# Kernel optimization log

Hardware: AMD Instinct MI355X
Metric: run time of the kernel (lower is better)

## Reference

```python
import jax, jax.numpy as jnp
import numpy as np

B, D_IN, D_PROJ, N_CLS = 4096, 4096, 1024, 32
N_CHILD = (32, 64)


def setup_inputs() -> dict:
    key = jax.random.key(0)
    ks = jax.random.split(key, 12)
    std = 2e-05
    inp = {
        "x": jax.random.normal(ks[0], (B, D_IN), dtype=jnp.float32),
        "y": jax.random.randint(ks[1], (B,), 0, N_CLS, dtype=jnp.int32),
        # parent projection: Linear(D_IN, D_PROJ)
        "Wp": jax.random.normal(ks[2], (D_IN, D_PROJ), dtype=jnp.float32) * std,
        "bp": jnp.zeros((D_PROJ,), jnp.float32),
        # subclass projection: Linear(D_IN, D_PROJ)
        "Ws": jax.random.normal(ks[3], (D_IN, D_PROJ), dtype=jnp.float32) * std,
        "bs": jnp.zeros((D_PROJ,), jnp.float32),
        # parent classifier: Linear(D_PROJ, N_CLS)
        "Wc": jax.random.normal(ks[4], (D_PROJ, N_CLS), dtype=jnp.float32) * std,
        "bc": jnp.zeros((N_CLS,), jnp.float32),
        # child expert banks: level i has N_CLS experts of Linear(D_PROJ, N_CHILD[i])
        "cw0": jax.random.normal(ks[5], (N_CLS, N_CHILD[0], D_PROJ), dtype=jnp.float32) * std,
        "cb0": jnp.zeros((N_CLS, N_CHILD[0]), jnp.float32),
        "cw1": jax.random.normal(ks[6], (N_CLS, N_CHILD[1], D_PROJ), dtype=jnp.float32) * std,
        "cb1": jnp.zeros((N_CLS, N_CHILD[1]), jnp.float32),
    }
    return inp


def reference(x, y, Wp, bp, Ws, bs, Wc, bc, cw0, cb0, cw1, cb1):
    # dropout p = 0.0 -> identity
    parent_proj_embed = x @ Wp + bp                 # [B, D_PROJ]
    parent_logits = parent_proj_embed @ Wc + bc     # [B, N_CLS]
    child_proj_embed = x @ Ws + bs                  # [B, D_PROJ]
    # per-sample expert routing: gather the expert for label y[b], then batched matvec
    child_logits0 = jnp.einsum("bd,bnd->bn", child_proj_embed, cw0[y]) + cb0[y]  # [B, 32]
    child_logits1 = jnp.einsum("bd,bnd->bn", child_proj_embed, cw1[y]) + cb1[y]  # [B, 64]
    return (parent_logits, child_logits0, child_logits1, parent_proj_embed, child_proj_embed)
```

## Files before the change

### kernel.cpp

```cpp
#include <hip/hip_runtime.h>
#include <hip/hip_bf16.h>
#include <stdint.h>


typedef __attribute__((ext_vector_type(4))) float  floatx4;
typedef __attribute__((ext_vector_type(8))) short  shortx8;
typedef __attribute__((ext_vector_type(4))) short  shortx4;
typedef __attribute__((ext_vector_type(8))) __bf16 bf16x8;

static __device__ __forceinline__ ushort f32_to_bf16_rne(float f) {
  uint32_t u = __builtin_bit_cast(uint32_t, f);
  u += 0x7FFFu + ((u >> 16) & 1u);
  return (ushort)(u >> 16);
}

static __device__ __forceinline__ void async_copy16(const void* g, void* lds) {
  __builtin_amdgcn_global_load_lds(
      (__attribute__((address_space(1))) void*)(uintptr_t)g,
      (__attribute__((address_space(3))) void*)(uintptr_t)lds,
      16, 0, 0);
}

__global__ __launch_bounds__(256) void k_prep(
    const float* __restrict__ x,   const int* __restrict__ y,
    const float* __restrict__ Wp,  const float* __restrict__ Ws,
    const float* __restrict__ Wc,
    const float* __restrict__ cw0, const float* __restrict__ cw1,
    ushort* __restrict__ xb,  ushort* __restrict__ Bt1,
    ushort* __restrict__ cwb, ushort* __restrict__ Wcb,
    int* __restrict__ perm, int* __restrict__ offs)
{
  __shared__ __align__(16) ushort tile[64 * 72];
  __shared__ int hist[32], hbase[32], hcur[32];
  const int b = blockIdx.x;
  const int t = threadIdx.x;

  if (b == 0) {
    if (t < 32) { hist[t] = 0; hcur[t] = 0; }
    __syncthreads();
    int yv[16];
    #pragma unroll
    for (int i = 0; i < 16; ++i) { yv[i] = y[t * 16 + i]; atomicAdd(&hist[yv[i]], 1); }
    __syncthreads();
    if (t == 0) {
      int s = 0;
      for (int c = 0; c < 32; ++c) { hbase[c] = s; offs[c] = s; s += hist[c]; }
      offs[32] = s;
    }
    __syncthreads();
    #pragma unroll
    for (int i = 0; i < 16; ++i) {
      const int c = yv[i];
      const int p = atomicAdd(&hcur[c], 1);
      perm[hbase[c] + p] = t * 16 + i;
    }
  } else if (b <= 4224) {
    const int row = b - 1;
    const int k = t * 4;
    float v0 = 0.f, v1 = 0.f, v2 = 0.f, v3 = 0.f;
    ushort* dst;
    if (row < 4096) {
      const int c = row >> 7, n = row & 127;
      if (n < 32) {
        floatx4 f = *reinterpret_cast<const floatx4*>(cw0 + (size_t)(c * 32 + n) * 1024 + k);
        v0 = f[0]; v1 = f[1]; v2 = f[2]; v3 = f[3];
      } else if (n < 96) {
        floatx4 f = *reinterpret_cast<const floatx4*>(cw1 + (size_t)(c * 64 + (n - 32)) * 1024 + k);
        v0 = f[0]; v1 = f[1]; v2 = f[2]; v3 = f[3];
      }
      dst = cwb + (size_t)row * 1024 + k;
    } else {
      const int n = row - 4096;
      if (n < 32) {
        v0 = Wc[(k + 0) * 32 + n]; v1 = Wc[(k + 1) * 32 + n];
        v2 = Wc[(k + 2) * 32 + n]; v3 = Wc[(k + 3) * 32 + n];
      }
      dst = Wcb + (size_t)n * 1024 + k;
    }
    shortx4 o;
    o[0] = (short)f32_to_bf16_rne(v0); o[1] = (short)f32_to_bf16_rne(v1);
    o[2] = (short)f32_to_bf16_rne(v2); o[3] = (short)f32_to_bf16_rne(v3);
    *reinterpret_cast<shortx4*>(dst) = o;
  } else if (b <= 6272) {
    const int vt = b - 4225;
    const int z = vt >> 10, rest = vt & 1023;
    const int nt = rest >> 6, kt = rest & 63;
    const float* W = z ? Ws : Wp;
    const int r = t >> 4, c = (t & 15) * 4;
    #pragma unroll
    for (int j = 0; j < 4; ++j) {
      const int kk = r + j * 16;
      floatx4 v = *reinterpret_cast<const floatx4*>(
          W + (size_t)(kt * 64 + kk) * 1024 + nt * 64 + c);
      tile[(c + 0) * 72 + kk] = f32_to_bf16_rne(v[0]);
      tile[(c + 1) * 72 + kk] = f32_to_bf16_rne(v[1]);
      tile[(c + 2) * 72 + kk] = f32_to_bf16_rne(v[2]);
      tile[(c + 3) * 72 + kk] = f32_to_bf16_rne(v[3]);
    }
    __syncthreads();
    const int nl = t >> 3, ch = t & 7;
    #pragma unroll
    for (int j = 0; j < 2; ++j) {
      const int n = nl + j * 32;
      shortx8 v = *reinterpret_cast<const shortx8*>(tile + n * 72 + ch * 8);
      *reinterpret_cast<shortx8*>(
          Bt1 + (size_t)(z * 1024 + nt * 64 + n) * 4096 + kt * 64 + ch * 8) = v;
    }
  } else {
    const size_t i = ((size_t)(b - 6273) * 256 + t) * 8;
    floatx4 a = *reinterpret_cast<const floatx4*>(x + i);
    floatx4 c = *reinterpret_cast<const floatx4*>(x + i + 4);
    shortx8 o;
    o[0] = (short)f32_to_bf16_rne(a[0]); o[1] = (short)f32_to_bf16_rne(a[1]);
    o[2] = (short)f32_to_bf16_rne(a[2]); o[3] = (short)f32_to_bf16_rne(a[3]);
    o[4] = (short)f32_to_bf16_rne(c[0]); o[5] = (short)f32_to_bf16_rne(c[1]);
    o[6] = (short)f32_to_bf16_rne(c[2]); o[7] = (short)f32_to_bf16_rne(c[3]);
    *reinterpret_cast<shortx8*>(xb + i) = o;
  }
}

__global__ __launch_bounds__(256) void k_gemm1(
    const ushort* __restrict__ xb, const ushort* __restrict__ Bt1,
    const float* __restrict__ bp, const float* __restrict__ bs,
    float* __restrict__ outP, float* __restrict__ outS,
    ushort* __restrict__ Pb, ushort* __restrict__ Sb)
{
  __shared__ __align__(16) ushort lA[128 * 128];
  __shared__ __align__(16) ushort lB[128 * 128];
  floatx4 acc[4][4];
  const floatx4 z4 = {0.f, 0.f, 0.f, 0.f};
  #pragma unroll
  for (int i = 0; i < 4; ++i)
    #pragma unroll
    for (int j = 0; j < 4; ++j) acc[i][j] = z4;

  const int t    = threadIdx.x;
  const int w    = t >> 6;
  const int lane = t & 63;
  const int wr   = w >> 1;
  const int wc   = w & 1;
  const int r16  = lane & 15;
  const int quad = lane >> 4;
  const int sr4  = lane >> 4;
  const int sc16 = lane & 15;

  const ushort* Abase = xb  + (size_t)(blockIdx.x * 128) * 4096;
  const ushort* Bbase = Bt1 + (size_t)(blockIdx.y * 128) * 4096;

  for (int k0 = 0; k0 < 4096; k0 += 128) {
    #pragma unroll
    for (int c2 = 0; c2 < 8; ++c2) {
      const int r  = 32 * w + 4 * c2 + sr4;
      const int gc = sc16 ^ (r & 15);
      async_copy16(Abase + (size_t)r * 4096 + k0 + gc * 8, lA + (32 * w + 4 * c2) * 128);
      async_copy16(Bbase + (size_t)r * 4096 + k0 + gc * 8, lB + (32 * w + 4 * c2) * 128);
    }
    __syncthreads();
    #pragma unroll
    for (int ks = 0; ks < 4; ++ks) {
      bf16x8 af[4], bfv[4];
      const int pc = (((ks * 4) + quad) ^ r16) * 8;
      #pragma unroll
      for (int mi = 0; mi < 4; ++mi)
        af[mi] = *reinterpret_cast<const bf16x8*>(lA + (wr * 64 + mi * 16 + r16) * 128 + pc);
      #pragma unroll
      for (int ni = 0; ni < 4; ++ni)
        bfv[ni] = *reinterpret_cast<const bf16x8*>(lB + (wc * 64 + ni * 16 + r16) * 128 + pc);
      #pragma unroll
      for (int mi = 0; mi < 4; ++mi)
        #pragma unroll
        for (int ni = 0; ni < 4; ++ni)
          acc[mi][ni] = __builtin_amdgcn_mfma_f32_16x16x32_bf16(
              af[mi], bfv[ni], acc[mi][ni], 0, 0, 0);
    }
    __syncthreads();
  }

  const int sel = (blockIdx.y >= 8);
  const float* bias = sel ? bs : bp;
  float*  outF = sel ? outS : outP;
  ushort* outB = sel ? Sb : Pb;
  const int colbase = blockIdx.y * 128 - sel * 1024;
  #pragma unroll
  for (int mi = 0; mi < 4; ++mi) {
    #pragma unroll
    for (int ni = 0; ni < 4; ++ni) {
      const int n = colbase + wc * 64 + ni * 16 + r16;
      const float bv = bias[n];
      #pragma unroll
      for (int rg = 0; rg < 4; ++rg) {
        const int m = blockIdx.x * 128 + wr * 64 + mi * 16 + quad * 4 + rg;
        const float v = acc[mi][ni][rg] + bv;
        const size_t off = (size_t)m * 1024 + n;
        outF[off] = v;
        outB[off] = f32_to_bf16_rne(v);
      }
    }
  }
}

static __device__ __forceinline__ void mfma_bk_step64(
    const ushort* lA, const ushort* lB, floatx4 acc[4][4],
    int wr, int wc, int r16, int quad)
{
  #pragma unroll
  for (int ks = 0; ks < 2; ++ks) {
    bf16x8 af[4], bfv[4];
    const int pc = (((ks * 4) + quad) ^ (r16 & 7)) * 8;
    #pragma unroll
    for (int mi = 0; mi < 4; ++mi)
      af[mi] = *reinterpret_cast<const bf16x8*>(lA + (wr * 64 + mi * 16 + r16) * 64 + pc);
    #pragma unroll
    for (int ni = 0; ni < 4; ++ni)
      bfv[ni] = *reinterpret_cast<const bf16x8*>(lB + (wc * 64 + ni * 16 + r16) * 64 + pc);
    #pragma unroll
    for (int mi = 0; mi < 4; ++mi)
      #pragma unroll
      for (int ni = 0; ni < 4; ++ni)
        acc[mi][ni] = __builtin_amdgcn_mfma_f32_16x16x32_bf16(
            af[mi], bfv[ni], acc[mi][ni], 0, 0, 0);
  }
}

__global__ __launch_bounds__(256) void k_head(
    const ushort* __restrict__ Sb, const ushort* __restrict__ Pb,
    const ushort* __restrict__ cwb, const ushort* __restrict__ Wcb,
    const int* __restrict__ perm, const int* __restrict__ off,
    const float* __restrict__ cb0, const float* __restrict__ cb1,
    const float* __restrict__ bc,
    float* __restrict__ out0, float* __restrict__ out1,
    float* __restrict__ outParent)
{
  __shared__ __align__(16) ushort lA[128 * 64];
  __shared__ __align__(16) ushort lB[128 * 64];
  floatx4 acc[4][4];
  const floatx4 z4 = {0.f, 0.f, 0.f, 0.f};
  #pragma unroll
  for (int i = 0; i < 4; ++i)
    #pragma unroll
    for (int j = 0; j < 4; ++j) acc[i][j] = z4;

  const int t = threadIdx.x, w = t >> 6, lane = t & 63;
  const int wr = w >> 1, wc = w & 1, r16 = lane & 15, quad = lane >> 4;
  const int sr = lane >> 3, sc = lane & 7;

  if (blockIdx.y == 32) {
    const ushort* Abase = Pb + (size_t)(blockIdx.x * 128) * 1024;
    for (int k0 = 0; k0 < 1024; k0 += 64) {
      #pragma unroll
      for (int c2 = 0; c2 < 4; ++c2) {
        const int r  = 32 * w + 8 * c2 + sr;
        const int gc = sc ^ sr;
        async_copy16(Abase + (size_t)r * 1024 + k0 + gc * 8, lA + (32 * w + 8 * c2) * 64);
        async_copy16(Wcb   + (size_t)r * 1024 + k0 + gc * 8, lB + (32 * w + 8 * c2) * 64);
      }
      __syncthreads();
      mfma_bk_step64(lA, lB, acc, wr, wc, r16, quad);
      __syncthreads();
    }
    if (wc == 0) {
      #pragma unroll
      for (int mi = 0; mi < 4; ++mi)
        #pragma unroll
        for (int ni = 0; ni < 2; ++ni) {
          const int n = ni * 16 + r16;
          const float bv = bc[n];
          #pragma unroll
          for (int rg = 0; rg < 4; ++rg) {
            const int m = blockIdx.x * 128 + wr * 64 + mi * 16 + quad * 4 + rg;
            outParent[(size_t)m * 32 + n] = acc[mi][ni][rg] + bv;
          }
        }
    }
    return;
  }

  const int c    = blockIdx.y;
  const int off0 = off[c];
  const int cnt  = off[c + 1] - off0;
  const int m0   = blockIdx.x * 128;
  if (m0 >= cnt) return;

  int rowSamp[4];
  #pragma unroll
  for (int c2 = 0; c2 < 4; ++c2) {
    const int r = 32 * w + 8 * c2 + sr;
    rowSamp[c2] = perm[off0 + min(m0 + r, cnt - 1)];
  }
  const ushort* Bbase = cwb + (size_t)c * 128 * 1024;

  for (int k0 = 0; k0 < 1024; k0 += 64) {
    #pragma unroll
    for (int c2 = 0; c2 < 4; ++c2) {
      const int r  = 32 * w + 8 * c2 + sr;
      const int gc = sc ^ sr;
      async_copy16(Sb + (size_t)rowSamp[c2] * 1024 + k0 + gc * 8, lA + (32 * w + 8 * c2) * 64);
      async_copy16(Bbase + (size_t)r * 1024 + k0 + gc * 8,        lB + (32 * w + 8 * c2) * 64);
    }
    __syncthreads();
    mfma_bk_step64(lA, lB, acc, wr, wc, r16, quad);
    __syncthreads();
  }

  #pragma unroll
  for (int mi = 0; mi < 4; ++mi) {
    #pragma unroll
    for (int rg = 0; rg < 4; ++rg) {
      const int gm = m0 + wr * 64 + mi * 16 + quad * 4 + rg;
      if (gm >= cnt) continue;
      const int sample = perm[off0 + gm];
      #pragma unroll
      for (int ni = 0; ni < 4; ++ni) {
        const int n = wc * 64 + ni * 16 + r16;
        if (n < 32)
          out0[(size_t)sample * 32 + n] = acc[mi][ni][rg] + cb0[c * 32 + n];
        else if (n < 96)
          out1[(size_t)sample * 64 + (n - 32)] = acc[mi][ni][rg] + cb1[c * 64 + (n - 32)];
      }
    }
  }
}


extern "C" void kernel_launch(void* const* d_in, const int* in_sizes, int n_in,
                              void* d_out, int out_size, void* d_ws, size_t ws_size,
                              hipStream_t stream) {
  const float* x   = (const float*)d_in[0];
  const int*   y   = (const int*)  d_in[1];
  const float* Wp  = (const float*)d_in[2];
  const float* bp  = (const float*)d_in[3];
  const float* Ws  = (const float*)d_in[4];
  const float* bs  = (const float*)d_in[5];
  const float* Wc  = (const float*)d_in[6];
  const float* bc  = (const float*)d_in[7];
  const float* cw0 = (const float*)d_in[8];
  const float* cb0 = (const float*)d_in[9];
  const float* cw1 = (const float*)d_in[10];
  const float* cb1 = (const float*)d_in[11];

  float* out = (float*)d_out;
  float* parent_logits = out;
  float* child0        = out + 131072;
  float* child1        = out + 262144;
  float* P             = out + 524288;
  float* S             = out + 4718592;

  char* ws = (char*)d_ws;
  ushort* xb   = (ushort*)(ws);
  ushort* Bt1  = (ushort*)(ws + 33554432);
  ushort* Pb   = (ushort*)(ws + 50331648);
  ushort* Sb   = (ushort*)(ws + 58720256);
  ushort* cwb  = (ushort*)(ws + 67108864);
  ushort* Wcb  = (ushort*)(ws + 75497472);
  int*    perm = (int*)   (ws + 75759616);
  int*    offs = (int*)   (ws + 75776000);

  k_prep <<<14465, 256, 0, stream>>>(x, y, Wp, Ws, Wc, cw0, cw1,
                                     xb, Bt1, cwb, Wcb, perm, offs);
  k_gemm1<<<dim3(32, 16), 256, 0, stream>>>(xb, Bt1, bp, bs, P, S, Pb, Sb);
  k_head <<<dim3(32, 33), 256, 0, stream>>>(Sb, Pb, cwb, Wcb, perm, offs,
                                            cb0, cb1, bc,
                                            child0, child1, parent_logits);
}
```

Before: 302.1 us.

## Pipeline GEMM1 with 4-slot async LDS ring and 256x128 tiles, 8 waves

Restructures the main projection GEMM to use 512-thread blocks computing 256x128 tiles with a BK=32, four-slot LDS ring buffer. Async global-to-LDS loads run three stages ahead and are gated by vmcnt waits with a single barrier per step, replacing the load-sync-compute-sync pattern. MFMA issue is wrapped in s_setprio. The aim is to hide global memory latency and raise B-tile reuse per block, at the cost of a smaller grid (256 blocks) and more register and LDS pressure.

```diff
diff --git a/kernel.cpp b/kernel.cpp
--- a/kernel.cpp
+++ b/kernel.cpp
@@ -119,14 +119,15 @@
   }
 }
 
-__global__ __launch_bounds__(256) void k_gemm1(
+__global__ __launch_bounds__(512, 2) void k_gemm1(
     const ushort* __restrict__ xb, const ushort* __restrict__ Bt1,
     const float* __restrict__ bp, const float* __restrict__ bs,
     float* __restrict__ outP, float* __restrict__ outS,
     ushort* __restrict__ Pb, ushort* __restrict__ Sb)
 {
-  __shared__ __align__(16) ushort lA[128 * 128];
-  __shared__ __align__(16) ushort lB[128 * 128];
+  __shared__ __align__(16) ushort lA[4 * 256 * 32];
+  __shared__ __align__(16) ushort lB[4 * 128 * 32];
+
   floatx4 acc[4][4];
   const floatx4 z4 = {0.f, 0.f, 0.f, 0.f};
   #pragma unroll
@@ -140,40 +141,67 @@
   const int wr   = w >> 1;
   const int wc   = w & 1;
   const int r16  = lane & 15;
-  const int quad = lane >> 4;
-  const int sr4  = lane >> 4;
-  const int sc16 = lane & 15;
-
-  const ushort* Abase = xb  + (size_t)(blockIdx.x * 128) * 4096;
+  const int qd   = lane >> 4;
+
+  const ushort* Abase = xb  + (size_t)(blockIdx.x * 256) * 4096;
   const ushort* Bbase = Bt1 + (size_t)(blockIdx.y * 128) * 4096;
 
-  for (int k0 = 0; k0 < 4096; k0 += 128) {
-    #pragma unroll
-    for (int c2 = 0; c2 < 8; ++c2) {
-      const int r  = 32 * w + 4 * c2 + sr4;
-      const int gc = sc16 ^ (r & 15);
-      async_copy16(Abase + (size_t)r * 4096 + k0 + gc * 8, lA + (32 * w + 4 * c2) * 128);
-      async_copy16(Bbase + (size_t)r * 4096 + k0 + gc * 8, lB + (32 * w + 4 * c2) * 128);
-    }
-    __syncthreads();
-    #pragma unroll
-    for (int ks = 0; ks < 4; ++ks) {
-      bf16x8 af[4], bfv[4];
-      const int pc = (((ks * 4) + quad) ^ r16) * 8;
-      #pragma unroll
-      for (int mi = 0; mi < 4; ++mi)
-        af[mi] = *reinterpret_cast<const bf16x8*>(lA + (wr * 64 + mi * 16 + r16) * 128 + pc);
+  const int    rA0  = t >> 2;
+  const int    qs   = ((t & 3) ^ (rA0 & 3)) << 3;
+  const size_t sA0  = (size_t)rA0 * 4096 + qs;
+  const size_t sA1  = (size_t)(128 + rA0) * 4096 + qs;
+  const size_t sB   = (size_t)rA0 * 4096 + qs;
+  const int    dUni = (t & ~63) * 8;
+
+  const int px  = qd ^ (r16 & 3);
+  const int aRd = (wr * 64 + r16) * 32 + px * 8;
+  const int bRd = (wc * 64 + r16) * 32 + px * 8;
+
+  #pragma unroll
+  for (int c = 0; c < 3; ++c) {
+    const int k0 = c * 32;
+    async_copy16(Abase + sA0 + k0, lA + c * 8192 + dUni);
+    async_copy16(Abase + sA1 + k0, lA + c * 8192 + 4096 + dUni);
+    async_copy16(Bbase + sB  + k0, lB + c * 4096 + dUni);
+  }
+  asm volatile("s_waitcnt vmcnt(6)" ::: "memory");
+  __builtin_amdgcn_s_barrier();
+  asm volatile("" ::: "memory");
+
+  for (int c = 0; c < 128; ++c) {
+    const int slot = c & 3;
+    const ushort* As = lA + slot * 8192;
+    const ushort* Bs = lB + slot * 4096;
+
+    bf16x8 af[4], bfv[4];
+    #pragma unroll
+    for (int mi = 0; mi < 4; ++mi)
+      af[mi] = *reinterpret_cast<const bf16x8*>(As + aRd + mi * 512);
+    #pragma unroll
+    for (int ni = 0; ni < 4; ++ni)
+      bfv[ni] = *reinterpret_cast<const bf16x8*>(Bs + bRd + ni * 512);
+
+    {
+      const int cs  = c + 3;
+      const int ss  = cs & 3;
+      const int k0s = (cs < 128 ? cs : 127) * 32;
+      async_copy16(Abase + sA0 + k0s, lA + ss * 8192 + dUni);
+      async_copy16(Abase + sA1 + k0s, lA + ss * 8192 + 4096 + dUni);
+      async_copy16(Bbase + sB  + k0s, lB + ss * 4096 + dUni);
+    }
+
+    __builtin_amdgcn_s_setprio(1);
+    #pragma unroll
+    for (int mi = 0; mi < 4; ++mi)
       #pragma unroll
       for (int ni = 0; ni < 4; ++ni)
-        bfv[ni] = *reinterpret_cast<const bf16x8*>(lB + (wc * 64 + ni * 16 + r16) * 128 + pc);
-      #pragma unroll
-      for (int mi = 0; mi < 4; ++mi)
-        #pragma unroll
-        for (int ni = 0; ni < 4; ++ni)
-          acc[mi][ni] = __builtin_amdgcn_mfma_f32_16x16x32_bf16(
-              af[mi], bfv[ni], acc[mi][ni], 0, 0, 0);
-    }
-    __syncthreads();
+        acc[mi][ni] = __builtin_amdgcn_mfma_f32_16x16x32_bf16(
+            af[mi], bfv[ni], acc[mi][ni], 0, 0, 0);
+    __builtin_amdgcn_s_setprio(0);
+
+    asm volatile("s_waitcnt vmcnt(6)" ::: "memory");
+    __builtin_amdgcn_s_barrier();
+    asm volatile("" ::: "memory");
   }
 
   const int sel = (blockIdx.y >= 8);
@@ -189,7 +217,7 @@
       const float bv = bias[n];
       #pragma unroll
       for (int rg = 0; rg < 4; ++rg) {
-        const int m = blockIdx.x * 128 + wr * 64 + mi * 16 + quad * 4 + rg;
+        const int m = blockIdx.x * 256 + wr * 64 + mi * 16 + qd * 4 + rg;
         const float v = acc[mi][ni][rg] + bv;
         const size_t off = (size_t)m * 1024 + n;
         outF[off] = v;
@@ -357,7 +385,7 @@
 
   k_prep <<<14465, 256, 0, stream>>>(x, y, Wp, Ws, Wc, cw0, cw1,
                                      xb, Bt1, cwb, Wcb, perm, offs);
-  k_gemm1<<<dim3(32, 16), 256, 0, stream>>>(xb, Bt1, bp, bs, P, S, Pb, Sb);
+  k_gemm1<<<dim3(16, 16), 512, 0, stream>>>(xb, Bt1, bp, bs, P, S, Pb, Sb);
   k_head <<<dim3(32, 33), 256, 0, stream>>>(Sb, Pb, cwb, Wcb, perm, offs,
                                             cb0, cb1, bc,
                                             child0, child1, parent_logits);
```

New measurement: 300.6 us. About the same (-0.5%).
